# Performance work log

Hardware: AMD Instinct MI355X
Metric: run time of the kernel (lower is better)

Reference implementation:

```python
import jax, jax.numpy as jnp
import numpy as np

DIM_EMB = 1024
NUM_HEADS = 16
DIM_HEAD = DIM_EMB // NUM_HEADS  # 64


def setup_inputs() -> dict:
    key = jax.random.key(0)
    k1, k2, k3 = jax.random.split(key, 3)
    x = jax.random.normal(k1, (4, 2048, DIM_EMB), dtype=jnp.float32)
    # nn.Linear(dim_embedding, 3*h*d, bias=False): weight shape [out, in]
    w_qkv = jax.random.normal(k2, (3 * NUM_HEADS * DIM_HEAD, DIM_EMB), dtype=jnp.float32) * (DIM_EMB ** -0.5)
    w_out = jax.random.normal(k3, (DIM_EMB, NUM_HEADS * DIM_HEAD), dtype=jnp.float32) * ((NUM_HEADS * DIM_HEAD) ** -0.5)
    return {"x": x, "w_qkv": w_qkv, "w_out": w_out}


def reference(x, w_qkv, w_out):
    b, t, _ = x.shape
    scale = DIM_HEAD ** -0.5
    qkv = jnp.einsum('bte,fe->btf', x, w_qkv)  # [b, t, 3*h*d]
    qkv = qkv.reshape(b, t, 3, NUM_HEADS, DIM_HEAD)  # fused dim order (k h d)
    q, k, v = qkv[:, :, 0], qkv[:, :, 1], qkv[:, :, 2]  # each [b, t, h, d]
    scores = jnp.einsum('bihd,bjhd->bhij', q, k) * scale  # [b, h, t, t]
    weights = jax.nn.softmax(scores, axis=-1)
    attn = jnp.einsum('bhij,bjhd->bhid', weights, v)  # [b, h, t, d]
    concat = attn.transpose(0, 2, 1, 3).reshape(b, t, NUM_HEADS * DIM_HEAD)
    return jnp.einsum('btf,ef->bte', concat, w_out)
```

## Files before the change

### kernel.cpp

```cpp
#include <hip/hip_runtime.h>

#define DI __device__ __forceinline__

typedef float  f32x2  __attribute__((ext_vector_type(2)));
typedef float  f32x4  __attribute__((ext_vector_type(4)));
typedef float  f32x16 __attribute__((ext_vector_type(16)));
typedef __bf16 bf16x8 __attribute__((ext_vector_type(8)));
typedef unsigned u32x2 __attribute__((ext_vector_type(2)));
typedef unsigned u32x4 __attribute__((ext_vector_type(4)));

static constexpr int TB   = 2048;
static constexpr int NTOK = 8192;
static constexpr int EMB  = 1024;
static constexpr int FQKV = 3072;

DI unsigned short f2bf(float f) {
  union { float f; unsigned u; } v; v.f = f;
  unsigned r = v.u + 0x7FFFu + ((v.u >> 16) & 1u);
  return (unsigned short)(r >> 16);
}

DI unsigned pack2bf(float a, float b) {
#if __has_builtin(__builtin_amdgcn_cvt_pk_bf16_f32)
  typedef __bf16 bf16x2 __attribute__((ext_vector_type(2)));
  bf16x2 r = __builtin_amdgcn_cvt_pk_bf16_f32(a, b);
  return __builtin_bit_cast(unsigned, r);
#else
  unsigned ua = __builtin_bit_cast(unsigned, a) + 0x8000u;
  unsigned ub = __builtin_bit_cast(unsigned, b) + 0x8000u;
  return __builtin_amdgcn_perm(ub, ua, 0x07060302u);
#endif
}

DI void plswap(unsigned& a, unsigned& b) {
#if __has_builtin(__builtin_amdgcn_permlane32_swap)
  u32x2 r = __builtin_amdgcn_permlane32_swap(a, b, false, false);
  a = r.x; b = r.y;
#else
  const bool hi = (threadIdx.x & 32) != 0;
  unsigned ax = (unsigned)__shfl_xor((int)a, 32);
  unsigned bx = (unsigned)__shfl_xor((int)b, 32);
  unsigned na = hi ? bx : a;
  unsigned nb = hi ? b : ax;
  a = na; b = nb;
#endif
}

DI bf16x8 frag4(unsigned a, unsigned b, unsigned c, unsigned d) {
  u32x4 u = {a, b, c, d};
  return __builtin_bit_cast(bf16x8, u);
}

DI void gload16(const void* g, void* l) {
  __builtin_amdgcn_global_load_lds(
      (__attribute__((address_space(1))) void*)(g),
      (__attribute__((address_space(3))) void*)(l), 16, 0, 0);
}

DI void syncdrain() {
  __builtin_amdgcn_s_waitcnt(0);
  __syncthreads();
}

__global__ __launch_bounds__(256)
void cvt_kernel(const float4* __restrict__ x, const float4* __restrict__ wq,
                const float4* __restrict__ wo,
                ushort4* __restrict__ xb, ushort4* __restrict__ wqb,
                ushort4* __restrict__ wob) {
  const int i  = blockIdx.x * 256 + threadIdx.x;
  const int nx = NTOK * EMB / 4;
  const int nq = FQKV * EMB / 4;
  float4 v; ushort4* dst;
  if (i < nx)           { v = x[i];           dst = xb  + i; }
  else if (i < nx + nq) { v = wq[i - nx];     dst = wqb + (i - nx); }
  else                  { v = wo[i - nx - nq]; dst = wob + (i - nx - nq); }
  ushort4 p;
  p.x = f2bf(v.x); p.y = f2bf(v.y); p.z = f2bf(v.z); p.w = f2bf(v.w);
  *dst = p;
}

template <int MODE>
__global__ __launch_bounds__(256)
void gemm_bt(const unsigned short* __restrict__ A,
             const unsigned short* __restrict__ Bt,
             const int K,
             unsigned short* __restrict__ qk,
             unsigned short* __restrict__ vT,
             float* __restrict__ outp) {
  __shared__ unsigned short sA[128 * 32];
  __shared__ unsigned short sB[128 * 32];
  const int tid  = threadIdx.x;
  const int w    = tid >> 6;
  const int l    = tid & 63;
  const int quad = l >> 4;
  const int lr   = l & 15;
  const int n0   = blockIdx.x * 128;
  const int m0   = blockIdx.y * 128;
  const int wm   = (w >> 1) * 64;
  const int wn   = (w & 1) * 64;

  f32x4 acc[4][4];
#pragma unroll
  for (int i = 0; i < 4; ++i)
#pragma unroll
    for (int j = 0; j < 4; ++j) acc[i][j] = {0.f, 0.f, 0.f, 0.f};

  const int srow = l >> 2;
  const int sg   = (l & 3) ^ ((l >> 3) & 3);
  const unsigned short* gA = A  + (long)(m0 + w * 32 + srow) * K + sg * 8;
  const unsigned short* gB = Bt + (long)(n0 + w * 32 + srow) * K + sg * 8;
  unsigned short* lA = sA + w * 1024;
  unsigned short* lB = sB + w * 1024;
  const int swz = (lr >> 1) & 3;

  for (int k0 = 0; k0 < K; k0 += 32) {
    gload16(gA + k0,          lA);
    gload16(gA + k0 + 16 * K, lA + 512);
    gload16(gB + k0,          lB);
    gload16(gB + k0 + 16 * K, lB + 512);
    syncdrain();
    bf16x8 af[4], bfr[4];
#pragma unroll
    for (int rt = 0; rt < 4; ++rt)
      af[rt] = *(const bf16x8*)(sA + (wm + rt * 16 + lr) * 32 + (quad ^ swz) * 8);
#pragma unroll
    for (int ct = 0; ct < 4; ++ct)
      bfr[ct] = *(const bf16x8*)(sB + (wn + ct * 16 + lr) * 32 + (quad ^ swz) * 8);
#pragma unroll
    for (int rt = 0; rt < 4; ++rt)
#pragma unroll
      for (int ct = 0; ct < 4; ++ct)
        acc[rt][ct] = __builtin_amdgcn_mfma_f32_16x16x32_bf16(af[rt], bfr[ct],
                                                              acc[rt][ct], 0, 0, 0);
    __syncthreads();
  }

  if (MODE == 0) {
    if (n0 < 2048) {
      const float qs = (n0 < 1024) ? 0.18033688011112042f : 1.0f;
#pragma unroll
      for (int rt = 0; rt < 4; ++rt) {
        const int row = m0 + wm + rt * 16 + quad * 4;
#pragma unroll
        for (int ct = 0; ct < 4; ++ct) {
          const int col = n0 + wn + ct * 16 + lr;
#pragma unroll
          for (int r = 0; r < 4; ++r)
            qk[(long)(row + r) * 2048 + col] = f2bf(acc[rt][ct][r] * qs);
        }
      }
    } else {
#pragma unroll
      for (int rt = 0; rt < 4; ++rt) {
        const int tok = m0 + wm + rt * 16 + quad * 4;
        const int bb  = tok >> 11, tt = tok & 2047;
#pragma unroll
        for (int ct = 0; ct < 4; ++ct) {
          const int fv = n0 - 2048 + wn + ct * 16 + lr;
          ushort4 p;
          p.x = f2bf(acc[rt][ct][0]); p.y = f2bf(acc[rt][ct][1]);
          p.z = f2bf(acc[rt][ct][2]); p.w = f2bf(acc[rt][ct][3]);
          *(ushort4*)(vT + ((long)(bb * 1024 + fv)) * 2048 + tt) = p;
        }
      }
    }
  } else {
#pragma unroll
    for (int rt = 0; rt < 4; ++rt) {
      const int row = m0 + wm + rt * 16 + quad * 4;
#pragma unroll
      for (int ct = 0; ct < 4; ++ct) {
        const int col = n0 + wn + ct * 16 + lr;
#pragma unroll
        for (int r = 0; r < 4; ++r)
          outp[(long)(row + r) * 1024 + col] = acc[rt][ct][r];
      }
    }
  }
}

__global__ __launch_bounds__(256)
void attn_kernel(const unsigned short* __restrict__ qk,
                 const unsigned short* __restrict__ vT,
                 unsigned short* __restrict__ attnb) {
  __shared__ unsigned short sK[2][64 * 64];
  __shared__ unsigned short sV[2][64 * 64];
  const int tid = threadIdx.x;
  const int w   = tid >> 6;
  const int l   = tid & 63;
  const int l31 = l & 31;
  const int lh  = l >> 5;
  const int h8  = lh * 8;
  const int bh  = blockIdx.x;
  const int hh  = bh & 15;
  const long tokbase = (long)(bh >> 4) * TB;
  const int qbase = blockIdx.y * 256 + w * 64;

  bf16x8 qf[2][4];
#pragma unroll
  for (int qs = 0; qs < 2; ++qs) {
    const unsigned short* qptr =
        qk + (tokbase + qbase + qs * 32 + l31) * 2048 + hh * 64 + h8;
#pragma unroll
    for (int s = 0; s < 4; ++s) qf[qs][s] = *(const bf16x8*)(qptr + s * 16);
  }

  const int srow = l >> 3;
  const int g    = (l & 7) ^ srow;
  const unsigned short* kbase =
      qk + (tokbase + w * 16 + srow) * 2048 + 1024 + hh * 64 + g * 8;
  const unsigned short* vbase =
      vT + ((long)bh * 64 + w * 16 + srow) * 2048 + g * 8;

  f32x16 oacc[2][2] = {{{}, {}}, {{}, {}}};
  f32x2 lp2[2] = {{0.f, 0.f}, {0.f, 0.f}};

  gload16(kbase,            &sK[0][(w * 16 + 0) * 64]);
  gload16(kbase + 8 * 2048, &sK[0][(w * 16 + 8) * 64]);
  gload16(vbase,            &sV[0][(w * 16 + 0) * 64]);
  gload16(vbase + 8 * 2048, &sV[0][(w * 16 + 8) * 64]);
  syncdrain();

  for (int t = 0; t < 32; ++t) {
    const int buf = t & 1;
    if (t + 1 < 32) {
      const int k0 = (t + 1) * 64;
      const int nb = buf ^ 1;
      gload16(kbase + (long)k0 * 2048,            &sK[nb][(w * 16 + 0) * 64]);
      gload16(kbase + (long)k0 * 2048 + 8 * 2048, &sK[nb][(w * 16 + 8) * 64]);
      gload16(vbase + k0,                         &sV[nb][(w * 16 + 0) * 64]);
      gload16(vbase + k0 + 8 * 2048,              &sV[nb][(w * 16 + 8) * 64]);
    }
    const unsigned short* bK = sK[buf];
    const unsigned short* bV = sV[buf];

#pragma unroll
    for (int G = 0; G < 2; ++G) {
      f32x16 sacc[2] = {{}, {}};
#pragma unroll
      for (int s = 0; s < 4; ++s) {
        const int key = G * 32 + l31;
        const int p   = (s * 2 + lh) ^ (key & 7);
        const bf16x8 kf = *(const bf16x8*)(bK + key * 64 + p * 8);
        sacc[0] = __builtin_amdgcn_mfma_f32_32x32x16_bf16(kf, qf[0][s], sacc[0], 0, 0, 0);
        sacc[1] = __builtin_amdgcn_mfma_f32_32x32x16_bf16(kf, qf[1][s], sacc[1], 0, 0, 0);
      }
      bf16x8 pp[2][2];
#pragma unroll
      for (int qs = 0; qs < 2; ++qs) {
        float e[16];
#pragma unroll
        for (int i = 0; i < 16; ++i) e[i] = __builtin_amdgcn_exp2f(sacc[qs][i]);
#pragma unroll
        for (int i = 0; i < 8; ++i) {
          f32x2 pr = {e[2 * i], e[2 * i + 1]};
          lp2[qs] += pr;
        }
        unsigned d[8];
#pragma unroll
        for (int i = 0; i < 8; ++i) d[i] = pack2bf(e[2 * i], e[2 * i + 1]);
        plswap(d[0], d[2]); plswap(d[1], d[3]);
        plswap(d[4], d[6]); plswap(d[5], d[7]);
        pp[qs][0] = frag4(d[0], d[1], d[2], d[3]);
        pp[qs][1] = frag4(d[4], d[5], d[6], d[7]);
      }
#pragma unroll
      for (int sub = 0; sub < 2; ++sub) {
        const int gt  = (G * 2 + sub) * 2 + lh;
        const int d0r = l31, d1r = 32 + l31;
        const bf16x8 vf0 = *(const bf16x8*)(bV + d0r * 64 + ((gt ^ (d0r & 7))) * 8);
        const bf16x8 vf1 = *(const bf16x8*)(bV + d1r * 64 + ((gt ^ (d1r & 7))) * 8);
#pragma unroll
        for (int qs = 0; qs < 2; ++qs) {
          oacc[qs][0] = __builtin_amdgcn_mfma_f32_32x32x16_bf16(pp[qs][sub], vf0, oacc[qs][0], 0, 0, 0);
          oacc[qs][1] = __builtin_amdgcn_mfma_f32_32x32x16_bf16(pp[qs][sub], vf1, oacc[qs][1], 0, 0, 0);
        }
      }
    }
    syncdrain();
  }

#pragma unroll
  for (int qs = 0; qs < 2; ++qs) {
    const float lp = lp2[qs].x + lp2[qs].y;
    const float fs = lp + __shfl_xor(lp, 32);
    const float rc = 1.0f / fs;
#pragma unroll
    for (int r = 0; r < 16; ++r) {
      const int row = (r & 3) + 8 * (r >> 2) + 4 * lh;
      const float sc = __shfl(rc, row);
      const long base = (tokbase + qbase + qs * 32 + row) * 1024 + hh * 64;
      attnb[base + l31]      = f2bf(oacc[qs][0][r] * sc);
      attnb[base + 32 + l31] = f2bf(oacc[qs][1][r] * sc);
    }
  }
}

extern "C" void kernel_launch(void* const* d_in, const int* in_sizes, int n_in,
                              void* d_out, int out_size, void* d_ws, size_t ws_size,
                              hipStream_t stream) {
  const float* x    = (const float*)d_in[0];
  const float* wqkv = (const float*)d_in[1];
  const float* wout = (const float*)d_in[2];
  float* outp = (float*)d_out;

  unsigned short* xb    = (unsigned short*)d_ws;
  unsigned short* wqkvb = xb    + (long)NTOK * EMB;
  unsigned short* woutb = wqkvb + (long)FQKV * EMB;
  unsigned short* qkb   = woutb + (long)EMB * EMB;
  unsigned short* vTb   = qkb   + (long)NTOK * 2048;
  unsigned short* attnb = vTb   + (long)4 * 16 * 64 * TB;

  cvt_kernel<<<12288, 256, 0, stream>>>(
      (const float4*)x, (const float4*)wqkv, (const float4*)wout,
      (ushort4*)xb, (ushort4*)wqkvb, (ushort4*)woutb);

  gemm_bt<0><<<dim3(24, 64), 256, 0, stream>>>(xb, wqkvb, EMB, qkb, vTb, nullptr);

  attn_kernel<<<dim3(64, 8), 256, 0, stream>>>(qkb, vTb, attnb);

  gemm_bt<1><<<dim3(8, 64), 256, 0, stream>>>(attnb, woutb, EMB, nullptr, nullptr, outp);
}
```

Baseline: 285.9 us.

## Halve per-warp query tile in attention to double grid and occupancy

Each wave in the attention kernel now handles 32 query rows instead of 64, so the grid doubles from 512 to 1024 blocks and launch bounds request 4 blocks per CU. This cuts accumulator and Q-fragment registers and should raise occupancy and load balance across CUs. The cost is that every K/V tile loaded into shared memory is reused by half as many query rows, which doubles total K/V global and LDS traffic. s_setprio hints are also added around the MFMA sections to favour matrix issue over the exp/pack work of other waves.

New measurement: 274.2 us. 4.1% less time.

```diff
diff --git a/kernel.cpp b/kernel.cpp
--- a/kernel.cpp
+++ b/kernel.cpp
@@ -179,7 +179,7 @@
   }
 }
 
-__global__ __launch_bounds__(256)
+__global__ __launch_bounds__(256, 4)
 void attn_kernel(const unsigned short* __restrict__ qk,
                  const unsigned short* __restrict__ vT,
                  unsigned short* __restrict__ attnb) {
@@ -194,15 +194,13 @@
   const int bh  = blockIdx.x;
   const int hh  = bh & 15;
   const long tokbase = (long)(bh >> 4) * TB;
-  const int qbase = blockIdx.y * 256 + w * 64;
-
-  bf16x8 qf[2][4];
-#pragma unroll
-  for (int qs = 0; qs < 2; ++qs) {
-    const unsigned short* qptr =
-        qk + (tokbase + qbase + qs * 32 + l31) * 2048 + hh * 64 + h8;
-#pragma unroll
-    for (int s = 0; s < 4; ++s) qf[qs][s] = *(const bf16x8*)(qptr + s * 16);
+  const int qbase = blockIdx.y * 128 + w * 32;
+
+  bf16x8 qf[4];
+  {
+    const unsigned short* qptr = qk + (tokbase + qbase + l31) * 2048 + hh * 64 + h8;
+#pragma unroll
+    for (int s = 0; s < 4; ++s) qf[s] = *(const bf16x8*)(qptr + s * 16);
   }
 
   const int srow = l >> 3;
@@ -212,8 +210,8 @@
   const unsigned short* vbase =
       vT + ((long)bh * 64 + w * 16 + srow) * 2048 + g * 8;
 
-  f32x16 oacc[2][2] = {{{}, {}}, {{}, {}}};
-  f32x2 lp2[2] = {{0.f, 0.f}, {0.f, 0.f}};
+  f32x16 oacc[2] = {{}, {}};
+  f32x2 lp2 = {0.f, 0.f};
 
   gload16(kbase,            &sK[0][(w * 16 + 0) * 64]);
   gload16(kbase + 8 * 2048, &sK[0][(w * 16 + 8) * 64]);
@@ -236,63 +234,57 @@
 
 #pragma unroll
     for (int G = 0; G < 2; ++G) {
-      f32x16 sacc[2] = {{}, {}};
+      f32x16 sacc = {};
+      __builtin_amdgcn_s_setprio(1);
 #pragma unroll
       for (int s = 0; s < 4; ++s) {
         const int key = G * 32 + l31;
         const int p   = (s * 2 + lh) ^ (key & 7);
         const bf16x8 kf = *(const bf16x8*)(bK + key * 64 + p * 8);
-        sacc[0] = __builtin_amdgcn_mfma_f32_32x32x16_bf16(kf, qf[0][s], sacc[0], 0, 0, 0);
-        sacc[1] = __builtin_amdgcn_mfma_f32_32x32x16_bf16(kf, qf[1][s], sacc[1], 0, 0, 0);
-      }
-      bf16x8 pp[2][2];
-#pragma unroll
-      for (int qs = 0; qs < 2; ++qs) {
-        float e[16];
-#pragma unroll
-        for (int i = 0; i < 16; ++i) e[i] = __builtin_amdgcn_exp2f(sacc[qs][i]);
-#pragma unroll
-        for (int i = 0; i < 8; ++i) {
-          f32x2 pr = {e[2 * i], e[2 * i + 1]};
-          lp2[qs] += pr;
-        }
-        unsigned d[8];
-#pragma unroll
-        for (int i = 0; i < 8; ++i) d[i] = pack2bf(e[2 * i], e[2 * i + 1]);
-        plswap(d[0], d[2]); plswap(d[1], d[3]);
-        plswap(d[4], d[6]); plswap(d[5], d[7]);
-        pp[qs][0] = frag4(d[0], d[1], d[2], d[3]);
-        pp[qs][1] = frag4(d[4], d[5], d[6], d[7]);
-      }
+        sacc = __builtin_amdgcn_mfma_f32_32x32x16_bf16(kf, qf[s], sacc, 0, 0, 0);
+      }
+      __builtin_amdgcn_s_setprio(0);
+      float e[16];
+#pragma unroll
+      for (int i = 0; i < 16; ++i) e[i] = __builtin_amdgcn_exp2f(sacc[i]);
+#pragma unroll
+      for (int i = 0; i < 8; ++i) {
+        f32x2 pr = {e[2 * i], e[2 * i + 1]};
+        lp2 += pr;
+      }
+      unsigned d[8];
+#pragma unroll
+      for (int i = 0; i < 8; ++i) d[i] = pack2bf(e[2 * i], e[2 * i + 1]);
+      plswap(d[0], d[2]); plswap(d[1], d[3]);
+      plswap(d[4], d[6]); plswap(d[5], d[7]);
+      bf16x8 pp[2];
+      pp[0] = frag4(d[0], d[1], d[2], d[3]);
+      pp[1] = frag4(d[4], d[5], d[6], d[7]);
+      __builtin_amdgcn_s_setprio(1);
 #pragma unroll
       for (int sub = 0; sub < 2; ++sub) {
         const int gt  = (G * 2 + sub) * 2 + lh;
         const int d0r = l31, d1r = 32 + l31;
         const bf16x8 vf0 = *(const bf16x8*)(bV + d0r * 64 + ((gt ^ (d0r & 7))) * 8);
         const bf16x8 vf1 = *(const bf16x8*)(bV + d1r * 64 + ((gt ^ (d1r & 7))) * 8);
-#pragma unroll
-        for (int qs = 0; qs < 2; ++qs) {
-          oacc[qs][0] = __builtin_amdgcn_mfma_f32_32x32x16_bf16(pp[qs][sub], vf0, oacc[qs][0], 0, 0, 0);
-          oacc[qs][1] = __builtin_amdgcn_mfma_f32_32x32x16_bf16(pp[qs][sub], vf1, oacc[qs][1], 0, 0, 0);
-        }
-      }
+        oacc[0] = __builtin_amdgcn_mfma_f32_32x32x16_bf16(pp[sub], vf0, oacc[0], 0, 0, 0);
+        oacc[1] = __builtin_amdgcn_mfma_f32_32x32x16_bf16(pp[sub], vf1, oacc[1], 0, 0, 0);
+      }
+      __builtin_amdgcn_s_setprio(0);
     }
     syncdrain();
   }
 
-#pragma unroll
-  for (int qs = 0; qs < 2; ++qs) {
-    const float lp = lp2[qs].x + lp2[qs].y;
-    const float fs = lp + __shfl_xor(lp, 32);
-    const float rc = 1.0f / fs;
-#pragma unroll
-    for (int r = 0; r < 16; ++r) {
-      const int row = (r & 3) + 8 * (r >> 2) + 4 * lh;
-      const float sc = __shfl(rc, row);
-      const long base = (tokbase + qbase + qs * 32 + row) * 1024 + hh * 64;
-      attnb[base + l31]      = f2bf(oacc[qs][0][r] * sc);
-      attnb[base + 32 + l31] = f2bf(oacc[qs][1][r] * sc);
-    }
+  const float lp = lp2.x + lp2.y;
+  const float fs = lp + __shfl_xor(lp, 32);
+  const float rc = 1.0f / fs;
+#pragma unroll
+  for (int r = 0; r < 16; ++r) {
+    const int row = (r & 3) + 8 * (r >> 2) + 4 * lh;
+    const float sc = __shfl(rc, row);
+    const long base = (tokbase + qbase + row) * 1024 + hh * 64;
+    attnb[base + l31]      = f2bf(oacc[0][r] * sc);
+    attnb[base + 32 + l31] = f2bf(oacc[1][r] * sc);
   }
 }
 
@@ -317,7 +309,7 @@
 
   gemm_bt<0><<<dim3(24, 64), 256, 0, stream>>>(xb, wqkvb, EMB, qkb, vTb, nullptr);
 
-  attn_kernel<<<dim3(64, 8), 256, 0, stream>>>(qkb, vTb, attnb);
+  attn_kernel<<<dim3(64, 16), 256, 0, stream>>>(qkb, vTb, attnb);
 
   gemm_bt<1><<<dim3(8, 64), 256, 0, stream>>>(attnb, woutb, EMB, nullptr, nullptr, outp);
 }
```
